# Kernel tuning notes

Measured on AMD Instinct MI355X. Metric: run time of the kernel, lower is better.

## Reference

```python
import jax, jax.numpy as jnp
import numpy as np

N, D = 4096, 2048

def setup_inputs() -> dict:
    key = jax.random.key(0)
    k1, k2 = jax.random.split(key)
    Ws = jax.random.normal(k1, (N, D), dtype=jnp.float32)
    # nn.Bilinear(D, D, 1): weight [1, D, D], bias [1]
    W = jax.random.normal(k2, (1, D, D), dtype=jnp.float32) * (1.0 / np.sqrt(D))
    b = jnp.zeros((1,), dtype=jnp.float32)
    return {"Ws": Ws, "W": W, "b": b}

def reference(Ws, W, b):
    # A[i, j] = Ws[i] @ W[0] @ Ws[j] + b[0]  (bilinear score for every pair)
    t = Ws @ W[0]                 # [N, D]
    A = t @ Ws.T + b[0]           # [N, N]
    return jax.nn.softmax(A, axis=1)
```

## Files before the change

kernel.cpp:

```cpp
#include <hip/hip_runtime.h>

typedef __bf16 bf16x8 __attribute__((ext_vector_type(8)));
typedef float f32x4 __attribute__((ext_vector_type(4)));
typedef unsigned short u16;
typedef u16 u16x8 __attribute__((ext_vector_type(8)));

#define AS1 __attribute__((address_space(1)))
#define AS3 __attribute__((address_space(3)))
#define MF(d, a, b) d = __builtin_amdgcn_mfma_f32_16x16x32_bf16(a, b, d, 0, 0, 0)

__device__ __forceinline__ void split2(float x, u16& h, u16& l) {
  __bf16 hb = (__bf16)x;
  float hf = (float)hb;
  __bf16 lb = (__bf16)(x - hf);
  h = __builtin_bit_cast(u16, hb);
  l = __builtin_bit_cast(u16, lb);
}

__global__ __launch_bounds__(256) void k_pack_ws(const float* __restrict__ X,
                                                 u16* __restrict__ P) {
  const int total8 = (4096 * 2048) / 8;
  for (int idx = blockIdx.x * 256 + threadIdx.x; idx < total8; idx += gridDim.x * 256) {
    int row = idx >> 8;
    int k8  = idx & 255;
    const float* src = X + ((size_t)row << 11) + (k8 << 3);
    const float4 v0 = *(const float4*)src;
    const float4 v1 = *(const float4*)(src + 4);
    float xv[8] = {v0.x, v0.y, v0.z, v0.w, v1.x, v1.y, v1.z, v1.w};
    u16x8 hv, lv;
#pragma unroll
    for (int j = 0; j < 8; ++j) { u16 h, l; split2(xv[j], h, l); hv[j] = h; lv[j] = l; }
    size_t base = ((size_t)row << 12) + (size_t)((k8 >> 2) << 6) + ((k8 & 3) << 3);
    *(u16x8*)(P + base) = hv;
    *(u16x8*)(P + base + 32) = lv;
  }
}

__global__ __launch_bounds__(256) void k_transpose_pack_w(const float* __restrict__ W,
                                                          u16* __restrict__ P) {
  __shared__ float tile[32][33];
  const int tx = threadIdx.x, ty = threadIdx.y;
  const int kbase = blockIdx.y << 5, cbase = blockIdx.x << 5;
#pragma unroll
  for (int i = 0; i < 4; ++i)
    tile[ty * 4 + i][tx] = W[((size_t)(kbase + ty * 4 + i) << 11) + cbase + tx];
  __syncthreads();
#pragma unroll
  for (int i = 0; i < 4; ++i) {
    int c = cbase + ty * 4 + i;
    float v = tile[tx][ty * 4 + i];
    u16 h, l; split2(v, h, l);
    size_t base = ((size_t)c << 12) + (size_t)(kbase << 1) + tx;
    P[base] = h;
    P[base + 32] = l;
  }
}

__global__ __launch_bounds__(256, 2) void k_gemm_nt(const u16* __restrict__ Ap,
                                                    const u16* __restrict__ Bp,
                                                    u16* __restrict__ Cpack) {
  __shared__ __align__(16) u16 lds_a[128 * 64];
  __shared__ __align__(16) u16 lds_b[128 * 64];
  const int bid = blockIdx.x;
  const int swzb = (bid & 7) * 64 + (bid >> 3);
  const int bx = swzb & 15, by = swzb >> 4;
  const int tid = threadIdx.x;
  const int lane = tid & 63, w = tid >> 6;
  const int wr = w >> 1, wc = w & 1;
  const int row0 = by << 7, col0 = bx << 7;
  const int lrow = lane & 15, kg = lane >> 4;

  f32x4 acc[4][4] = {};

  const u16* abase = Ap + ((size_t)row0 << 12);
  const u16* bbase = Bp + ((size_t)col0 << 12);

  int offAh[4], offAl[4], offBh[4], offBl[4];
#pragma unroll
  for (int m = 0; m < 4; ++m) {
    int r = wr * 64 + m * 16 + lrow;
    int sw = r & 7;
    offAh[m] = r * 64 + ((kg ^ sw) << 3);
    offAl[m] = r * 64 + (((4 + kg) ^ sw) << 3);
    int rb = wc * 64 + m * 16 + lrow;
    int swb = rb & 7;
    offBh[m] = rb * 64 + ((kg ^ swb) << 3);
    offBl[m] = rb * 64 + (((4 + kg) ^ swb) << 3);
  }

  for (int kb = 0; kb < 64; ++kb) {
    const int kofs = kb << 6;
#pragma unroll
    for (int i = 0; i < 4; ++i) {
      int s = i * 256 + tid;
      int r = s >> 3, c = s & 7;
      int cs = c ^ (r & 7);
      __builtin_amdgcn_global_load_lds(
          (const AS1 unsigned int*)(abase + ((size_t)r << 12) + kofs + (cs << 3)),
          (AS3 unsigned int*)(lds_a + ((i * 256 + w * 64) << 3)), 16, 0, 0);
    }
#pragma unroll
    for (int i = 0; i < 4; ++i) {
      int s = i * 256 + tid;
      int r = s >> 3, c = s & 7;
      int cs = c ^ (r & 7);
      __builtin_amdgcn_global_load_lds(
          (const AS1 unsigned int*)(bbase + ((size_t)r << 12) + kofs + (cs << 3)),
          (AS3 unsigned int*)(lds_b + ((i * 256 + w * 64) << 3)), 16, 0, 0);
    }
    __syncthreads();

    bf16x8 ah[4], al[4];
#pragma unroll
    for (int m = 0; m < 4; ++m) {
      ah[m] = *(const bf16x8*)&lds_a[offAh[m]];
      al[m] = *(const bf16x8*)&lds_a[offAl[m]];
    }
#pragma unroll
    for (int n = 0; n < 4; ++n) {
      bf16x8 bh = *(const bf16x8*)&lds_b[offBh[n]];
      bf16x8 bl = *(const bf16x8*)&lds_b[offBl[n]];
#pragma unroll
      for (int m = 0; m < 4; ++m) {
        MF(acc[m][n], ah[m], bh);
        MF(acc[m][n], ah[m], bl);
        MF(acc[m][n], al[m], bh);
      }
    }
    __syncthreads();
  }

#pragma unroll
  for (int m = 0; m < 4; ++m) {
#pragma unroll
    for (int n = 0; n < 4; ++n) {
#pragma unroll
      for (int j = 0; j < 4; ++j) {
        int gr = row0 + wr * 64 + m * 16 + kg * 4 + j;
        int gc = col0 + wc * 64 + n * 16 + lrow;
        u16 h, l; split2(acc[m][n][j], h, l);
        size_t base = ((size_t)gr << 12) + (size_t)((gc >> 5) << 6) + (gc & 31);
        Cpack[base] = h;
        Cpack[base + 32] = l;
      }
    }
  }
}

__global__ __launch_bounds__(512, 2) void k_gemm256(const u16* __restrict__ Ap,
                                                    const u16* __restrict__ Bp,
                                                    float* __restrict__ Cout) {
  __shared__ __align__(16) u16 sm[65536];
  const int bid = blockIdx.x;
  const int swzb = (bid & 7) * 32 + (bid >> 3);
  const int bx = swzb & 15, by = swzb >> 4;
  const int tid = threadIdx.x;
  const int lane = tid & 63, w = tid >> 6;
  const int wr = w >> 2, wc = w & 3;
  const int row0 = by << 8, col0 = bx << 8;
  const int lrow = lane & 15, kg = lane >> 4;
  const int sw = lrow & 7;

  const u16* Abase = Ap + ((size_t)row0 << 12);
  const u16* Bbase = Bp + ((size_t)col0 << 12);

  const size_t gsrc0 = ((size_t)(tid >> 3) << 12) + ((size_t)((tid & 7) ^ ((tid >> 3) & 7)) << 3);
  const int dst0 = (w * 64) << 3;

  auto stA = [&](int T, int j) {
    __builtin_amdgcn_global_load_lds(
        (const AS1 unsigned int*)(Abase + gsrc0 + ((size_t)(j * 64) << 12) + ((T & 63) << 6)),
        (AS3 unsigned int*)(sm + ((T & 1) << 14) + j * 4096 + dst0), 16, 0, 0);
  };
  auto stB = [&](int T, int j) {
    __builtin_amdgcn_global_load_lds(
        (const AS1 unsigned int*)(Bbase + gsrc0 + ((size_t)(j * 64) << 12) + ((T & 63) << 6)),
        (AS3 unsigned int*)(sm + 32768 + ((T & 1) << 14) + j * 4096 + dst0), 16, 0, 0);
  };

  const int baseAh = (wr * 128 + lrow) * 64 + ((kg ^ sw) << 3);
  const int baseAl = (wr * 128 + lrow) * 64 + (((4 | kg) ^ sw) << 3);
  const int baseBh = (wc * 64 + lrow) * 64 + ((kg ^ sw) << 3);
  const int baseBl = (wc * 64 + lrow) * 64 + (((4 | kg) ^ sw) << 3);

  f32x4 acc[8][4] = {};
  bf16x8 bh[4], bl[4];

  stA(0, 0); stA(0, 1); stA(0, 2); stA(0, 3);
  stB(0, 0); stB(0, 1); stB(0, 2); stB(0, 3);
  stB(1, 0); stB(1, 1); stB(1, 2); stB(1, 3);
  stA(1, 0); stA(1, 2);
  asm volatile("s_waitcnt vmcnt(6)" ::: "memory");
  __builtin_amdgcn_sched_barrier(0);
  __builtin_amdgcn_s_barrier();

  for (int i = 0; i < 32; ++i) {
    const int t0 = 2 * i;
#pragma unroll
    for (int p = 0; p < 8; ++p) {
      const int q = p & 3;
      const int t = t0 + (p >> 2);
      const u16* la = sm + ((t & 1) << 14);
      const u16* lb = sm + 32768 + ((t & 1) << 14);
      if (q == 0) {
#pragma unroll
        for (int n = 0; n < 4; ++n) {
          bh[n] = *(const bf16x8*)&lb[baseBh + n * 1024];
          bl[n] = *(const bf16x8*)&lb[baseBl + n * 1024];
        }
      }
      bf16x8 ah0 = *(const bf16x8*)&la[baseAh + (2 * q) * 1024];
      bf16x8 al0 = *(const bf16x8*)&la[baseAl + (2 * q) * 1024];
      bf16x8 ah1 = *(const bf16x8*)&la[baseAh + (2 * q + 1) * 1024];
      bf16x8 al1 = *(const bf16x8*)&la[baseAl + (2 * q + 1) * 1024];
      switch (p) {
        case 0: stA(t0 + 1, 1); stA(t0 + 1, 3); break;
        case 1: stB(t0 + 2, 0); stB(t0 + 2, 1); break;
        case 2: stB(t0 + 2, 2); stB(t0 + 2, 3); break;
        case 3: stA(t0 + 2, 0); stA(t0 + 2, 2); break;
        case 4: stA(t0 + 2, 1); stA(t0 + 2, 3); break;
        case 5: stB(t0 + 3, 0); stB(t0 + 3, 1); break;
        case 6: stB(t0 + 3, 2); stB(t0 + 3, 3); break;
        case 7: stA(t0 + 3, 0); stA(t0 + 3, 2); break;
      }
      __builtin_amdgcn_s_barrier();
      __builtin_amdgcn_s_setprio(1);
      const int m0 = 2 * q, m1 = 2 * q + 1;
#pragma unroll
      for (int n = 0; n < 4; ++n) { MF(acc[m0][n], ah0, bh[n]); MF(acc[m1][n], ah1, bh[n]); }
#pragma unroll
      for (int n = 0; n < 4; ++n) { MF(acc[m0][n], ah0, bl[n]); MF(acc[m1][n], ah1, bl[n]); }
#pragma unroll
      for (int n = 0; n < 4; ++n) { MF(acc[m0][n], al0, bh[n]); MF(acc[m1][n], al1, bh[n]); }
      __builtin_amdgcn_s_setprio(0);
      asm volatile("s_waitcnt lgkmcnt(0)" ::: "memory");
      __builtin_amdgcn_sched_barrier(0);
      if (q == 3) {
        asm volatile("s_waitcnt vmcnt(6)" ::: "memory");
        __builtin_amdgcn_sched_barrier(0);
      }
      __builtin_amdgcn_s_barrier();
    }
  }
  asm volatile("s_waitcnt vmcnt(0)" ::: "memory");

#pragma unroll
  for (int m = 0; m < 8; ++m) {
#pragma unroll
    for (int n = 0; n < 4; ++n) {
#pragma unroll
      for (int j = 0; j < 4; ++j) {
        int gr = row0 + wr * 128 + m * 16 + kg * 4 + j;
        int gc = col0 + wc * 64 + n * 16 + lrow;
        Cout[((size_t)gr << 12) + gc] = acc[m][n][j];
      }
    }
  }
}

__global__ __launch_bounds__(256) void k_softmax_rows(float* __restrict__ A) {
  const int row = blockIdx.x;
  float* p = A + ((size_t)row << 12);
  const int tid = threadIdx.x;
  const int lane = tid & 63, w = tid >> 6;
  float4 v[4];
  float mx = -3.0e38f;
#pragma unroll
  for (int i = 0; i < 4; ++i) {
    v[i] = ((const float4*)p)[tid + (i << 8)];
    mx = fmaxf(mx, fmaxf(fmaxf(v[i].x, v[i].y), fmaxf(v[i].z, v[i].w)));
  }
#pragma unroll
  for (int off = 32; off; off >>= 1) mx = fmaxf(mx, __shfl_xor(mx, off, 64));
  __shared__ float redm[4], reds[4];
  if (lane == 0) redm[w] = mx;
  __syncthreads();
  mx = fmaxf(fmaxf(redm[0], redm[1]), fmaxf(redm[2], redm[3]));
  float s = 0.f;
#pragma unroll
  for (int i = 0; i < 4; ++i) {
    v[i].x = __expf(v[i].x - mx);
    v[i].y = __expf(v[i].y - mx);
    v[i].z = __expf(v[i].z - mx);
    v[i].w = __expf(v[i].w - mx);
    s += (v[i].x + v[i].y) + (v[i].z + v[i].w);
  }
#pragma unroll
  for (int off = 32; off; off >>= 1) s += __shfl_xor(s, off, 64);
  if (lane == 0) reds[w] = s;
  __syncthreads();
  s = (reds[0] + reds[1]) + (reds[2] + reds[3]);
  const float inv = 1.0f / s;
#pragma unroll
  for (int i = 0; i < 4; ++i) {
    v[i].x *= inv; v[i].y *= inv; v[i].z *= inv; v[i].w *= inv;
    ((float4*)p)[tid + (i << 8)] = v[i];
  }
}

extern "C" void kernel_launch(void* const* d_in, const int* in_sizes, int n_in,
                              void* d_out, int out_size, void* d_ws, size_t ws_size,
                              hipStream_t stream) {
  (void)in_sizes; (void)n_in; (void)out_size; (void)ws_size;
  const float* Ws = (const float*)d_in[0];
  const float* W  = (const float*)d_in[1];
  float* out = (float*)d_out;

  u16* ws_pack = (u16*)d_ws;
  u16* wt_pack = ws_pack + (size_t)4096 * 4096;
  u16* t_pack  = wt_pack + (size_t)2048 * 4096;

  k_pack_ws<<<4096, 256, 0, stream>>>(Ws, ws_pack);
  k_transpose_pack_w<<<dim3(64, 64), dim3(32, 8), 0, stream>>>(W, wt_pack);
  k_gemm_nt<<<512, 256, 0, stream>>>(ws_pack, wt_pack, t_pack);
  k_gemm256<<<256, 512, 0, stream>>>(t_pack, ws_pack, out);
  k_softmax_rows<<<4096, 256, 0, stream>>>(out);
}
```

Measured before the change: 261.3 us.

## Double-buffer B fragments in registers and spread their LDS reads across phases

The B-operand register fragments for the next K tile are now loaded early, spread over several sub-phases, into a second register set (even/odd), instead of all at once at the start of each tile. This spreads LDS read traffic and hides its latency behind MFMA work. An extra vmcnt wait is added at phases 0 and 4 so the odd/even B tile is resident before its early reads. This costs 32 extra VGPRs for the second B set, which can raise register pressure or cause spills, and the added wait may stall.

Result: no change. 263.5 us (+0.9%).

```diff
diff --git a/kernel.cpp b/kernel.cpp
--- a/kernel.cpp
+++ b/kernel.cpp
@@ -183,8 +183,13 @@
   const int baseBh = (wc * 64 + lrow) * 64 + ((kg ^ sw) << 3);
   const int baseBl = (wc * 64 + lrow) * 64 + (((4 | kg) ^ sw) << 3);
 
+  const u16* laE = sm;
+  const u16* laO = sm + 16384;
+  const u16* lbE = sm + 32768;
+  const u16* lbO = sm + 49152;
+
   f32x4 acc[8][4] = {};
-  bf16x8 bh[4], bl[4];
+  bf16x8 bhE[4], blE[4], bhO[4], blO[4];
 
   stA(0, 0); stA(0, 1); stA(0, 2); stA(0, 3);
   stB(0, 0); stB(0, 1); stB(0, 2); stB(0, 3);
@@ -193,26 +198,41 @@
   asm volatile("s_waitcnt vmcnt(6)" ::: "memory");
   __builtin_amdgcn_sched_barrier(0);
   __builtin_amdgcn_s_barrier();
+#pragma unroll
+  for (int n = 0; n < 4; ++n) {
+    bhE[n] = *(const bf16x8*)&lbE[baseBh + n * 1024];
+    blE[n] = *(const bf16x8*)&lbE[baseBl + n * 1024];
+  }
 
   for (int i = 0; i < 32; ++i) {
     const int t0 = 2 * i;
 #pragma unroll
     for (int p = 0; p < 8; ++p) {
       const int q = p & 3;
-      const int t = t0 + (p >> 2);
-      const u16* la = sm + ((t & 1) << 14);
-      const u16* lb = sm + 32768 + ((t & 1) << 14);
-      if (q == 0) {
-#pragma unroll
-        for (int n = 0; n < 4; ++n) {
-          bh[n] = *(const bf16x8*)&lb[baseBh + n * 1024];
-          bl[n] = *(const bf16x8*)&lb[baseBl + n * 1024];
-        }
-      }
+      const u16* la = (p < 4) ? laE : laO;
       bf16x8 ah0 = *(const bf16x8*)&la[baseAh + (2 * q) * 1024];
       bf16x8 al0 = *(const bf16x8*)&la[baseAl + (2 * q) * 1024];
       bf16x8 ah1 = *(const bf16x8*)&la[baseAh + (2 * q + 1) * 1024];
       bf16x8 al1 = *(const bf16x8*)&la[baseAl + (2 * q + 1) * 1024];
+      switch (p) {
+        case 1: bhO[0] = *(const bf16x8*)&lbO[baseBh];
+                blO[0] = *(const bf16x8*)&lbO[baseBl];
+                bhO[1] = *(const bf16x8*)&lbO[baseBh + 1024]; break;
+        case 2: blO[1] = *(const bf16x8*)&lbO[baseBl + 1024];
+                bhO[2] = *(const bf16x8*)&lbO[baseBh + 2048];
+                blO[2] = *(const bf16x8*)&lbO[baseBl + 2048]; break;
+        case 3: bhO[3] = *(const bf16x8*)&lbO[baseBh + 3072];
+                blO[3] = *(const bf16x8*)&lbO[baseBl + 3072]; break;
+        case 5: bhE[0] = *(const bf16x8*)&lbE[baseBh];
+                blE[0] = *(const bf16x8*)&lbE[baseBl];
+                bhE[1] = *(const bf16x8*)&lbE[baseBh + 1024]; break;
+        case 6: blE[1] = *(const bf16x8*)&lbE[baseBl + 1024];
+                bhE[2] = *(const bf16x8*)&lbE[baseBh + 2048];
+                blE[2] = *(const bf16x8*)&lbE[baseBl + 2048]; break;
+        case 7: bhE[3] = *(const bf16x8*)&lbE[baseBh + 3072];
+                blE[3] = *(const bf16x8*)&lbE[baseBl + 3072]; break;
+        default: break;
+      }
       switch (p) {
         case 0: stA(t0 + 1, 1); stA(t0 + 1, 3); break;
         case 1: stB(t0 + 2, 0); stB(t0 + 2, 1); break;
@@ -226,16 +246,29 @@
       __builtin_amdgcn_s_barrier();
       __builtin_amdgcn_s_setprio(1);
       const int m0 = 2 * q, m1 = 2 * q + 1;
-#pragma unroll
-      for (int n = 0; n < 4; ++n) { MF(acc[m0][n], ah0, bh[n]); MF(acc[m1][n], ah1, bh[n]); }
-#pragma unroll
-      for (int n = 0; n < 4; ++n) { MF(acc[m0][n], ah0, bl[n]); MF(acc[m1][n], ah1, bl[n]); }
-#pragma unroll
-      for (int n = 0; n < 4; ++n) { MF(acc[m0][n], al0, bh[n]); MF(acc[m1][n], al1, bh[n]); }
+      if (p < 4) {
+#pragma unroll
+        for (int n = 0; n < 4; ++n) { MF(acc[m0][n], ah0, bhE[n]); MF(acc[m1][n], ah1, bhE[n]); }
+#pragma unroll
+        for (int n = 0; n < 4; ++n) { MF(acc[m0][n], ah0, blE[n]); MF(acc[m1][n], ah1, blE[n]); }
+#pragma unroll
+        for (int n = 0; n < 4; ++n) { MF(acc[m0][n], al0, bhE[n]); MF(acc[m1][n], al1, bhE[n]); }
+      } else {
+#pragma unroll
+        for (int n = 0; n < 4; ++n) { MF(acc[m0][n], ah0, bhO[n]); MF(acc[m1][n], ah1, bhO[n]); }
+#pragma unroll
+        for (int n = 0; n < 4; ++n) { MF(acc[m0][n], ah0, blO[n]); MF(acc[m1][n], ah1, blO[n]); }
+#pragma unroll
+        for (int n = 0; n < 4; ++n) { MF(acc[m0][n], al0, bhO[n]); MF(acc[m1][n], al1, bhO[n]); }
+      }
       __builtin_amdgcn_s_setprio(0);
       asm volatile("s_waitcnt lgkmcnt(0)" ::: "memory");
       __builtin_amdgcn_sched_barrier(0);
-      if (q == 3) {
+      if (p == 0 || p == 4) {
+        asm volatile("s_waitcnt vmcnt(4)" ::: "memory");
+        __builtin_amdgcn_sched_barrier(0);
+      }
+      if (p == 3 || p == 7) {
         asm volatile("s_waitcnt vmcnt(6)" ::: "memory");
         __builtin_amdgcn_sched_barrier(0);
       }
```
